# Performance work log

Hardware: AMD Instinct MI355X
Metric: run time of the kernel (lower is better)

The kernel has to match this reference:

```python
import jax, jax.numpy as jnp
import numpy as np

NUM_HEADS = 16
NUM_HIDDENS = 1024
D_K = NUM_HIDDENS // NUM_HEADS
NEG_INF = -1.0e9


def setup_inputs() -> dict:
    key = jax.random.key(0)
    kx, kq, kk, kv, ko, kl = jax.random.split(key, 6)
    B, S, D = 2, 2048, NUM_HIDDENS
    scale = 1.0 / np.sqrt(D)
    return {
        "X": jax.random.normal(kx, (B, S, D), dtype=jnp.float32),
        "valid_lens": jax.random.randint(kl, (B,), 0, S, dtype=jnp.int64),
        "W_q": jax.random.normal(kq, (D, D), dtype=jnp.float32) * scale,
        "W_k": jax.random.normal(kk, (D, D), dtype=jnp.float32) * scale,
        "W_v": jax.random.normal(kv, (D, D), dtype=jnp.float32) * scale,
        "W_o": jax.random.normal(ko, (D, D), dtype=jnp.float32) * scale,
    }


def _split_heads(x):
    # [B, S, D] -> [B, H, S, d_k]
    B, S, _ = x.shape
    return x.reshape(B, S, NUM_HEADS, D_K).transpose(0, 2, 1, 3)


def reference(X, valid_lens, W_q, W_k, W_v, W_o):
    B, S, D = X.shape
    # nn.Linear(bias=False): y = x @ W.T  (W is [out, in])
    Q = _split_heads(jnp.einsum("bsd,ed->bse", X, W_q))  # [B,H,S,dk]
    K = _split_heads(jnp.einsum("bsd,ed->bse", X, W_k))
    V = _split_heads(jnp.einsum("bsd,ed->bse", X, W_v))

    scores = jnp.einsum("bhqd,bhkd->bhqk", Q, K) / jnp.sqrt(
        jnp.asarray(D_K, dtype=X.dtype)
    )  # [B,H,S,S]

    # key-position mask per batch: positions >= valid_len get -1e9
    mask = jnp.arange(S)[None, :] >= valid_lens[:, None]  # [B,S]
    scores = jnp.where(mask[:, None, None, :], jnp.asarray(NEG_INF, X.dtype), scores)

    attn = jax.nn.softmax(scores, axis=-1)  # dropout p=0 -> identity
    out = jnp.einsum("bhqk,bhkd->bhqd", attn, V)  # [B,H,S,dk]
    out = out.transpose(0, 2, 1, 3).reshape(B, S, D)
    return jnp.einsum("bsd,ed->bse", out, W_o)
```

## Files before the change

kernel.cpp:

```cpp
#include <hip/hip_runtime.h>
#include <stdint.h>

#define S_LEN 2048
#define BATCH 2
#define DMODEL 1024
#define NHEAD 16
#define DK 64
#define MROWS (BATCH * S_LEN)

typedef __attribute__((ext_vector_type(8))) short bf16x8;
typedef __attribute__((ext_vector_type(4))) float f32x4;
typedef __attribute__((ext_vector_type(4))) short short4v;
typedef __attribute__((ext_vector_type(2))) uint32_t u32x2;

__device__ __forceinline__ short f2b(float f) {
    union { float f; uint32_t u; } c; c.f = f;
    uint32_t u = c.u;
    return (short)((u + 0x7fffu + ((u >> 16) & 1u)) >> 16);
}

__device__ __forceinline__ void gload16(const void* g, void* l) {
    __builtin_amdgcn_global_load_lds(
        (const __attribute__((address_space(1))) void*)g,
        (__attribute__((address_space(3))) void*)l, 16, 0, 0);
}

__global__ void cvt_kernel(const float* __restrict__ X, const float* __restrict__ Wq,
                           const float* __restrict__ Wk, const float* __restrict__ Wv,
                           const float* __restrict__ Wo,
                           short* __restrict__ Xb, short* __restrict__ Wqb,
                           short* __restrict__ Wkb, short* __restrict__ Wvb,
                           short* __restrict__ Wob) {
    const float* src; short* dst; int n4;
    switch (blockIdx.y) {
        case 0:  src = X;  dst = Xb;  n4 = MROWS * DMODEL / 4;  break;
        case 1:  src = Wq; dst = Wqb; n4 = DMODEL * DMODEL / 4; break;
        case 2:  src = Wk; dst = Wkb; n4 = DMODEL * DMODEL / 4; break;
        case 3:  src = Wv; dst = Wvb; n4 = DMODEL * DMODEL / 4; break;
        default: src = Wo; dst = Wob; n4 = DMODEL * DMODEL / 4; break;
    }
    for (int i = blockIdx.x * blockDim.x + threadIdx.x; i < n4;
         i += gridDim.x * blockDim.x) {
        float4 v = ((const float4*)src)[i];
        short4v o;
        o[0] = f2b(v.x); o[1] = f2b(v.y); o[2] = f2b(v.z); o[3] = f2b(v.w);
        ((short4v*)dst)[i] = o;
    }
}

template <int OUT_F32>
__global__ __launch_bounds__(256) void gemm_bt(
    const short* __restrict__ A,
    const short* __restrict__ Bt0, const short* __restrict__ Bt1,
    const short* __restrict__ Bt2,
    short* __restrict__ Cb0, short* __restrict__ Cb1, short* __restrict__ Cb2,
    float* __restrict__ Cf, int M, int N, int K) {
    __shared__ short sA[128 * 32];
    __shared__ short sB[128 * 32];

    const short* Bt = Bt0;
    short* Cb = Cb0;
    if (blockIdx.z == 1) { Bt = Bt1; Cb = Cb1; }
    else if (blockIdx.z == 2) { Bt = Bt2; Cb = Cb2; }

    const int tid = threadIdx.x;
    const int lane = tid & 63;
    const int wid = tid >> 6;
    const int wr = wid >> 1, wc = wid & 1;
    const int brow = blockIdx.y * 128;
    const int bcol = blockIdx.x * 128;
    const int lr = lane & 15;
    const int kh = (lane >> 4) << 3;

    f32x4 acc[4][4] = {};

    const int idx0 = tid, idx1 = tid + 256;
    const int ar0 = idx0 >> 2, ak0 = (idx0 & 3) << 3;
    const int ar1 = idx1 >> 2, ak1 = (idx1 & 3) << 3;

    const int nk = K >> 5;
    for (int kt = 0; kt < nk; ++kt) {
        __syncthreads();
        const int k0 = kt << 5;
        gload16(A + (size_t)(brow + ar0) * K + k0 + ak0, &sA[idx0 * 8]);
        gload16(A + (size_t)(brow + ar1) * K + k0 + ak1, &sA[idx1 * 8]);
        gload16(Bt + (size_t)(bcol + ar0) * K + k0 + ak0, &sB[idx0 * 8]);
        gload16(Bt + (size_t)(bcol + ar1) * K + k0 + ak1, &sB[idx1 * 8]);
        __syncthreads();

        bf16x8 a[4], b[4];
#pragma unroll
        for (int mt = 0; mt < 4; ++mt)
            a[mt] = *(const bf16x8*)&sA[(wr * 64 + mt * 16 + lr) * 32 + kh];
#pragma unroll
        for (int nt = 0; nt < 4; ++nt)
            b[nt] = *(const bf16x8*)&sB[(wc * 64 + nt * 16 + lr) * 32 + kh];
#pragma unroll
        for (int mt = 0; mt < 4; ++mt)
#pragma unroll
            for (int nt = 0; nt < 4; ++nt)
                acc[mt][nt] = __builtin_amdgcn_mfma_f32_16x16x32_bf16(
                    a[mt], b[nt], acc[mt][nt], 0, 0, 0);
    }

    const int rbase = (lane >> 4) << 2;
    const bool vtrans = (!OUT_F32) && (blockIdx.z == 2);
#pragma unroll
    for (int mt = 0; mt < 4; ++mt) {
#pragma unroll
        for (int nt = 0; nt < 4; ++nt) {
            if (vtrans) {
                int row0 = brow + wr * 64 + mt * 16 + rbase;
                int col = bcol + wc * 64 + nt * 16 + lr;
                int bb = row0 >> 11, key = row0 & 2047;
                int hh = col >> 6, d = col & 63;
                short4v pk;
#pragma unroll
                for (int j = 0; j < 4; ++j) pk[j] = f2b(acc[mt][nt][j]);
                *(short4v*)&Cb[((size_t)((bb * 16 + hh) * 64 + d)) * S_LEN + key] = pk;
            } else {
#pragma unroll
                for (int j = 0; j < 4; ++j) {
                    int row = brow + wr * 64 + mt * 16 + rbase + j;
                    int col = bcol + wc * 64 + nt * 16 + lr;
                    if (OUT_F32)
                        Cf[(size_t)row * N + col] = acc[mt][nt][j];
                    else
                        Cb[(size_t)row * N + col] = f2b(acc[mt][nt][j]);
                }
            }
        }
    }
}

__global__ __launch_bounds__(256) void attn_kernel(
    const short* __restrict__ Q, const short* __restrict__ K,
    const short* __restrict__ Vt, short* __restrict__ O,
    const int* __restrict__ vlens) {
    __shared__ short sK[2][64 * 64];
    __shared__ short sV[2][64 * 64];
    __shared__ short sP[4][16 * 64];

    const int tid = threadIdx.x;
    const int lane = tid & 63;
    const int w = tid >> 6;
    const int id = blockIdx.x;
    const int id2 = ((id & 7) << 7) | (id >> 3);
    const int qb = id2 & 31;
    const int bhx = id2 >> 5;
    const int b = bhx & 1, h = bhx >> 1;
    const int lr = lane & 15;
    const int kh = (lane >> 4) << 3;
    const int rbase = (lane >> 4) << 2;
    const int swq = (lr & 7) << 3;

    int vl = vlens[b];
    if (vl < 0) vl = 0;
    if (vl > S_LEN) vl = S_LEN;
    const bool allm = (vl == 0);
    if (allm) vl = S_LEN;
    const int nT = (vl + 63) >> 6;
    const int nFull = ((vl & 63) == 0) ? nT : nT - 1;

    const size_t rowbase = (size_t)(b * S_LEN) * DMODEL + h * DK;
    const short* vt = Vt + ((size_t)((b * 16 + h) * 64)) * S_LEN;

    const short* qrow = Q + rowbase + (size_t)(qb * 64 + w * 16 + lr) * DMODEL;
    bf16x8 qf0 = *(const bf16x8*)(qrow + kh);
    bf16x8 qf1 = *(const bf16x8*)(qrow + 32 + kh);
    if (allm) {
#pragma unroll
        for (int i = 0; i < 8; ++i) { qf0[i] = 0; qf1[i] = 0; }
    }

    f32x4 oac[4] = {};
    float m_run = -1e30f, m_c = -1e30f, l_run = 0.f;
    const float CEXP = 0.18033688011112042f;
    const float THRADD = 44.361419556f;

    const int lofs0 = lr * 64 + (kh ^ swq);
    const int lofs1 = lr * 64 + ((32 + kh) ^ swq);

    const int kr0 = tid >> 3;
    const int kr1 = kr0 + 32;
    const int kc0 = (((tid & 7) ^ (kr0 & 7)) << 3);
    const int kc1 = (((tid & 7) ^ (kr1 & 7)) << 3);

    const short* kA = K + rowbase + (size_t)kr0 * DMODEL + kc0;
    const short* kB = K + rowbase + (size_t)kr1 * DMODEL + kc1;
    const short* vA = vt + (size_t)kr0 * S_LEN + kc0;
    const short* vB = vt + (size_t)kr1 * S_LEN + kc1;

    gload16(kA, &sK[0][tid * 8]);
    gload16(kB, &sK[0][(tid + 256) * 8]);
    gload16(vA, &sV[0][tid * 8]);
    gload16(vB, &sV[0][(tid + 256) * 8]);
    __syncthreads();

#define TILE_BODY(MASKED_C)                                                     \
    do {                                                                        \
        constexpr bool MASKED = MASKED_C;                                       \
        const short* sKc = sK[cur];                                             \
        const short* sVc = sV[cur];                                             \
        const short* kL0 = sKc + lofs0;                                         \
        const short* kL1 = sKc + lofs1;                                         \
        f32x4 sacc[4] = {};                                                     \
        __builtin_amdgcn_s_setprio(1);                                          \
        _Pragma("unroll")                                                       \
        for (int nt = 0; nt < 4; ++nt) {                                        \
            bf16x8 kb0 = *(const bf16x8*)&kL0[nt * 1024];                       \
            bf16x8 kb1 = *(const bf16x8*)&kL1[nt * 1024];                       \
            sacc[nt] = __builtin_amdgcn_mfma_f32_16x16x32_bf16(                 \
                kb0, qf0, sacc[nt], 0, 0, 0);                                   \
            sacc[nt] = __builtin_amdgcn_mfma_f32_16x16x32_bf16(                 \
                kb1, qf1, sacc[nt], 0, 0, 0);                                   \
        }                                                                       \
        __builtin_amdgcn_s_setprio(0);                                          \
        if (MASKED) {                                                           \
            _Pragma("unroll")                                                   \
            for (int nt = 0; nt < 4; ++nt)                                      \
                _Pragma("unroll")                                               \
                for (int j = 0; j < 4; ++j) {                                   \
                    int keyi = t * 64 + nt * 16 + rbase + j;                    \
                    if (keyi >= vl) sacc[nt][j] = -3.0e38f;                     \
                }                                                               \
        }                                                                       \
        float t0 = fmaxf(fmaxf(sacc[0][0], sacc[0][1]), sacc[0][2]);            \
        float t1 = fmaxf(fmaxf(sacc[0][3], sacc[1][0]), sacc[1][1]);            \
        float t2 = fmaxf(fmaxf(sacc[1][2], sacc[1][3]), sacc[2][0]);            \
        float t3 = fmaxf(fmaxf(sacc[2][1], sacc[2][2]), sacc[2][3]);            \
        float t4 = fmaxf(fmaxf(sacc[3][0], sacc[3][1]), sacc[3][2]);            \
        float pmax = fmaxf(fmaxf(fmaxf(t0, t1), t2),                            \
                           fmaxf(fmaxf(t3, t4), sacc[3][3]));                   \
        if (__any(pmax > m_run + THRADD)) {                                     \
            float mx = pmax;                                                    \
            mx = fmaxf(mx, __shfl_xor(mx, 16));                                 \
            mx = fmaxf(mx, __shfl_xor(mx, 32));                                 \
            float scl = __builtin_exp2f((m_run - mx) * CEXP);                   \
            m_run = mx;                                                         \
            m_c = mx * CEXP;                                                    \
            l_run *= scl;                                                       \
            _Pragma("unroll")                                                   \
            for (int dt = 0; dt < 4; ++dt)                                      \
                _Pragma("unroll")                                               \
                for (int j = 0; j < 4; ++j) oac[dt][j] *= scl;                  \
        }                                                                       \
        float p[16];                                                            \
        _Pragma("unroll")                                                       \
        for (int nt = 0; nt < 4; ++nt)                                          \
            _Pragma("unroll")                                                   \
            for (int j = 0; j < 4; ++j)                                         \
                p[nt * 4 + j] = __builtin_exp2f(                                \
                    __builtin_fmaf(sacc[nt][j], CEXP, -m_c));                   \
        float ls = ((p[0] + p[1]) + (p[2] + p[3])) +                            \
                   ((p[4] + p[5]) + (p[6] + p[7]));                             \
        ls += ((p[8] + p[9]) + (p[10] + p[11])) +                               \
              ((p[12] + p[13]) + (p[14] + p[15]));                              \
        l_run += ls;                                                            \
        _Pragma("unroll")                                                       \
        for (int nt = 0; nt < 4; ++nt) {                                        \
            u32x2 r;                                                            \
            asm("v_cvt_pk_bf16_f32 %0, %1, %2"                                  \
                : "=v"(r[0]) : "v"(p[nt * 4 + 0]), "v"(p[nt * 4 + 1]));         \
            asm("v_cvt_pk_bf16_f32 %0, %1, %2"                                  \
                : "=v"(r[1]) : "v"(p[nt * 4 + 2]), "v"(p[nt * 4 + 3]));         \
            *(u32x2*)&sP[w][lr * 64 + ((nt * 16 + rbase) ^ swq)] = r;           \
        }                                                                       \
        const short* pL0 = &sP[w][lofs0];                                       \
        const short* pL1 = &sP[w][lofs1];                                       \
        const short* vL0 = sVc + lofs0;                                         \
        const short* vL1 = sVc + lofs1;                                         \
        __builtin_amdgcn_s_setprio(1);                                          \
        {                                                                       \
            bf16x8 pf0 = *(const bf16x8*)pL0;                                   \
            _Pragma("unroll")                                                   \
            for (int dt = 0; dt < 4; ++dt) {                                    \
                bf16x8 vf = *(const bf16x8*)&vL0[dt * 1024];                    \
                oac[dt] = __builtin_amdgcn_mfma_f32_16x16x32_bf16(              \
                    vf, pf0, oac[dt], 0, 0, 0);                                 \
            }                                                                   \
            bf16x8 pf1 = *(const bf16x8*)pL1;                                   \
            _Pragma("unroll")                                                   \
            for (int dt = 0; dt < 4; ++dt) {                                    \
                bf16x8 vf = *(const bf16x8*)&vL1[dt * 1024];                    \
                oac[dt] = __builtin_amdgcn_mfma_f32_16x16x32_bf16(              \
                    vf, pf1, oac[dt], 0, 0, 0);                                 \
            }                                                                   \
        }                                                                       \
        __builtin_amdgcn_s_setprio(0);                                          \
    } while (0)

    int cur = 0;
    for (int t = 0; t < nT; ++t) {
        const bool hn = (t + 1 < nT);
        if (hn) {
            short* sKn = sK[cur ^ 1];
            short* sVn = sV[cur ^ 1];
            kA += 64 * DMODEL; kB += 64 * DMODEL;
            vA += 64; vB += 64;
            gload16(kA, &sKn[tid * 8]);
            gload16(kB, &sKn[(tid + 256) * 8]);
            gload16(vA, &sVn[tid * 8]);
            gload16(vB, &sVn[(tid + 256) * 8]);
        }

        if (t < nFull) TILE_BODY(false);
        else TILE_BODY(true);

        __syncthreads();
        cur ^= 1;
    }
#undef TILE_BODY

    float lt = l_run + __shfl_xor(l_run, 16);
    lt += __shfl_xor(lt, 32);
    float rl = 1.f / lt;

    short* orow = O + rowbase + (size_t)(qb * 64 + w * 16 + lr) * DMODEL;
#pragma unroll
    for (int dt = 0; dt < 4; ++dt) {
        short4v pk;
#pragma unroll
        for (int j = 0; j < 4; ++j) pk[j] = f2b(oac[dt][j] * rl);
        *(short4v*)&orow[dt * 16 + rbase] = pk;
    }
}

extern "C" void kernel_launch(void* const* d_in, const int* in_sizes, int n_in,
                              void* d_out, int out_size, void* d_ws, size_t ws_size,
                              hipStream_t stream) {
    const float* X = (const float*)d_in[0];
    const int* vlens = (const int*)d_in[1];
    const float* Wq = (const float*)d_in[2];
    const float* Wk = (const float*)d_in[3];
    const float* Wv = (const float*)d_in[4];
    const float* Wo = (const float*)d_in[5];
    float* out = (float*)d_out;

    short* Xb = (short*)d_ws;
    short* Wqb = Xb + (size_t)MROWS * DMODEL;
    short* Wkb = Wqb + (size_t)DMODEL * DMODEL;
    short* Wvb = Wkb + (size_t)DMODEL * DMODEL;
    short* Wob = Wvb + (size_t)DMODEL * DMODEL;
    short* Qb = Wob + (size_t)DMODEL * DMODEL;
    short* Kb = Qb + (size_t)MROWS * DMODEL;
    short* Vtb = Kb + (size_t)MROWS * DMODEL;
    short* Ob = Vtb + (size_t)MROWS * DMODEL;

    cvt_kernel<<<dim3(512, 5), 256, 0, stream>>>(X, Wq, Wk, Wv, Wo, Xb, Wqb, Wkb,
                                                 Wvb, Wob);
    gemm_bt<0><<<dim3(8, 32, 3), 256, 0, stream>>>(Xb, Wqb, Wkb, Wvb, Qb, Kb, Vtb,
                                                   nullptr, MROWS, DMODEL, DMODEL);
    attn_kernel<<<dim3(1024), 256, 0, stream>>>(Qb, Kb, Vtb, Ob, vlens);
    gemm_bt<1><<<dim3(8, 32, 1), 256, 0, stream>>>(Ob, Wob, Wob, Wob, nullptr,
                                                   nullptr, nullptr, out, MROWS,
                                                   DMODEL, DMODEL);
}
```

Baseline: 119.7 us.

## Process 32 query rows per wave in attention and swizzle GEMM LDS

The attention kernel now gives each wave two 16-row query fragments, so every K and V tile loaded into LDS feeds twice as many MFMAs, and the grid is halved to 512 blocks. Softmax logic moves into a macro applied to both fragments, with separate running max/sum state and a doubled P buffer. Separately, the GEMM LDS layout gets an XOR swizzle on the k-offset to reduce bank conflicts on fragment reads. The cost is higher register pressure and fewer blocks for the 256 CUs, which may leave some idle or hurt load balance across varying valid lengths.

```diff
diff --git a/kernel.cpp b/kernel.cpp
--- a/kernel.cpp
+++ b/kernel.cpp
@@ -71,12 +71,14 @@
     const int bcol = blockIdx.x * 128;
     const int lr = lane & 15;
     const int kh = (lane >> 4) << 3;
+    const int swg = ((lr >> 1) & 3) << 3;
+    const int khs = kh ^ swg;
 
     f32x4 acc[4][4] = {};
 
     const int idx0 = tid, idx1 = tid + 256;
-    const int ar0 = idx0 >> 2, ak0 = (idx0 & 3) << 3;
-    const int ar1 = idx1 >> 2, ak1 = (idx1 & 3) << 3;
+    const int ar0 = idx0 >> 2, ak0 = ((idx0 & 3) << 3) ^ (((ar0 >> 1) & 3) << 3);
+    const int ar1 = idx1 >> 2, ak1 = ((idx1 & 3) << 3) ^ (((ar1 >> 1) & 3) << 3);
 
     const int nk = K >> 5;
     for (int kt = 0; kt < nk; ++kt) {
@@ -91,10 +93,10 @@
         bf16x8 a[4], b[4];
 #pragma unroll
         for (int mt = 0; mt < 4; ++mt)
-            a[mt] = *(const bf16x8*)&sA[(wr * 64 + mt * 16 + lr) * 32 + kh];
+            a[mt] = *(const bf16x8*)&sA[(wr * 64 + mt * 16 + lr) * 32 + khs];
 #pragma unroll
         for (int nt = 0; nt < 4; ++nt)
-            b[nt] = *(const bf16x8*)&sB[(wc * 64 + nt * 16 + lr) * 32 + kh];
+            b[nt] = *(const bf16x8*)&sB[(wc * 64 + nt * 16 + lr) * 32 + khs];
 #pragma unroll
         for (int mt = 0; mt < 4; ++mt)
 #pragma unroll
@@ -139,15 +141,15 @@
     const int* __restrict__ vlens) {
     __shared__ short sK[2][64 * 64];
     __shared__ short sV[2][64 * 64];
-    __shared__ short sP[4][16 * 64];
+    __shared__ short sP[4][2][16 * 64];
 
     const int tid = threadIdx.x;
     const int lane = tid & 63;
     const int w = tid >> 6;
     const int id = blockIdx.x;
-    const int id2 = ((id & 7) << 7) | (id >> 3);
-    const int qb = id2 & 31;
-    const int bhx = id2 >> 5;
+    const int id2 = ((id & 7) << 6) | (id >> 3);
+    const int qb = id2 & 15;
+    const int bhx = id2 >> 4;
     const int b = bhx & 1, h = bhx >> 1;
     const int lr = lane & 15;
     const int kh = (lane >> 4) << 3;
@@ -165,16 +167,20 @@
     const size_t rowbase = (size_t)(b * S_LEN) * DMODEL + h * DK;
     const short* vt = Vt + ((size_t)((b * 16 + h) * 64)) * S_LEN;
 
-    const short* qrow = Q + rowbase + (size_t)(qb * 64 + w * 16 + lr) * DMODEL;
-    bf16x8 qf0 = *(const bf16x8*)(qrow + kh);
-    bf16x8 qf1 = *(const bf16x8*)(qrow + 32 + kh);
+    const short* qrowA = Q + rowbase + (size_t)(qb * 128 + w * 32 + lr) * DMODEL;
+    const short* qrowB = qrowA + 16 * DMODEL;
+    bf16x8 qf0a = *(const bf16x8*)(qrowA + kh);
+    bf16x8 qf1a = *(const bf16x8*)(qrowA + 32 + kh);
+    bf16x8 qf0b = *(const bf16x8*)(qrowB + kh);
+    bf16x8 qf1b = *(const bf16x8*)(qrowB + 32 + kh);
     if (allm) {
 #pragma unroll
-        for (int i = 0; i < 8; ++i) { qf0[i] = 0; qf1[i] = 0; }
-    }
-
-    f32x4 oac[4] = {};
-    float m_run = -1e30f, m_c = -1e30f, l_run = 0.f;
+        for (int i = 0; i < 8; ++i) { qf0a[i] = 0; qf1a[i] = 0; qf0b[i] = 0; qf1b[i] = 0; }
+    }
+
+    f32x4 oacA[4] = {}, oacB[4] = {};
+    float mA = -1e30f, mcA = -1e30f, lA = 0.f;
+    float mB = -1e30f, mcB = -1e30f, lB = 0.f;
     const float CEXP = 0.18033688011112042f;
     const float THRADD = 44.361419556f;
 
@@ -196,6 +202,51 @@
     gload16(vA, &sV[0][tid * 8]);
     gload16(vB, &sV[0][(tid + 256) * 8]);
     __syncthreads();
+
+#define SOFTMAX_FRAG(SACC, MRUN, MC, LRUN, OAC, SPW)                            \
+    do {                                                                        \
+        float t0 = fmaxf(fmaxf(SACC[0][0], SACC[0][1]), SACC[0][2]);            \
+        float t1 = fmaxf(fmaxf(SACC[0][3], SACC[1][0]), SACC[1][1]);            \
+        float t2 = fmaxf(fmaxf(SACC[1][2], SACC[1][3]), SACC[2][0]);            \
+        float t3 = fmaxf(fmaxf(SACC[2][1], SACC[2][2]), SACC[2][3]);            \
+        float t4 = fmaxf(fmaxf(SACC[3][0], SACC[3][1]), SACC[3][2]);            \
+        float pmax = fmaxf(fmaxf(fmaxf(t0, t1), t2),                            \
+                           fmaxf(fmaxf(t3, t4), SACC[3][3]));                   \
+        if (__any(pmax > MRUN + THRADD)) {                                      \
+            float mx = pmax;                                                    \
+            mx = fmaxf(mx, __shfl_xor(mx, 16));                                 \
+            mx = fmaxf(mx, __shfl_xor(mx, 32));                                 \
+            float scl = __builtin_exp2f((MRUN - mx) * CEXP);                    \
+            MRUN = mx;                                                          \
+            MC = mx * CEXP;                                                     \
+            LRUN *= scl;                                                        \
+            _Pragma("unroll")                                                   \
+            for (int dt = 0; dt < 4; ++dt)                                      \
+                _Pragma("unroll")                                               \
+                for (int j = 0; j < 4; ++j) OAC[dt][j] *= scl;                  \
+        }                                                                       \
+        float p[16];                                                            \
+        _Pragma("unroll")                                                       \
+        for (int nt = 0; nt < 4; ++nt)                                          \
+            _Pragma("unroll")                                                   \
+            for (int j = 0; j < 4; ++j)                                         \
+                p[nt * 4 + j] = __builtin_exp2f(                                \
+                    __builtin_fmaf(SACC[nt][j], CEXP, -MC));                    \
+        float ls = ((p[0] + p[1]) + (p[2] + p[3])) +                            \
+                   ((p[4] + p[5]) + (p[6] + p[7]));                             \
+        ls += ((p[8] + p[9]) + (p[10] + p[11])) +                               \
+              ((p[12] + p[13]) + (p[14] + p[15]));                              \
+        LRUN += ls;                                                             \
+        _Pragma("unroll")                                                       \
+        for (int nt = 0; nt < 4; ++nt) {                                        \
+            u32x2 r;                                                            \
+            asm("v_cvt_pk_bf16_f32 %0, %1, %2"                                  \
+                : "=v"(r[0]) : "v"(p[nt * 4 + 0]), "v"(p[nt * 4 + 1]));         \
+            asm("v_cvt_pk_bf16_f32 %0, %1, %2"                                  \
+                : "=v"(r[1]) : "v"(p[nt * 4 + 2]), "v"(p[nt * 4 + 3]));         \
+            *(u32x2*)&SPW[lr * 64 + ((nt * 16 + rbase) ^ swq)] = r;             \
+        }                                                                       \
+    } while (0)
 
 #define TILE_BODY(MASKED_C)                                                     \
     do {                                                                        \
@@ -204,16 +255,20 @@
         const short* sVc = sV[cur];                                             \
         const short* kL0 = sKc + lofs0;                                         \
         const short* kL1 = sKc + lofs1;                                         \
-        f32x4 sacc[4] = {};                                                     \
+        f32x4 saccA[4] = {}, saccB[4] = {};                                     \
         __builtin_amdgcn_s_setprio(1);                                          \
         _Pragma("unroll")                                                       \
         for (int nt = 0; nt < 4; ++nt) {                                        \
             bf16x8 kb0 = *(const bf16x8*)&kL0[nt * 1024];                       \
             bf16x8 kb1 = *(const bf16x8*)&kL1[nt * 1024];                       \
-            sacc[nt] = __builtin_amdgcn_mfma_f32_16x16x32_bf16(                 \
-                kb0, qf0, sacc[nt], 0, 0, 0);                                   \
-            sacc[nt] = __builtin_amdgcn_mfma_f32_16x16x32_bf16(                 \
-                kb1, qf1, sacc[nt], 0, 0, 0);                                   \
+            saccA[nt] = __builtin_amdgcn_mfma_f32_16x16x32_bf16(                \
+                kb0, qf0a, saccA[nt], 0, 0, 0);                                 \
+            saccB[nt] = __builtin_amdgcn_mfma_f32_16x16x32_bf16(                \
+                kb0, qf0b, saccB[nt], 0, 0, 0);                                 \
+            saccA[nt] = __builtin_amdgcn_mfma_f32_16x16x32_bf16(                \
+                kb1, qf1a, saccA[nt], 0, 0, 0);                                 \
+            saccB[nt] = __builtin_amdgcn_mfma_f32_16x16x32_bf16(                \
+                kb1, qf1b, saccB[nt], 0, 0, 0);                                 \
         }                                                                       \
         __builtin_amdgcn_s_setprio(0);                                          \
         if (MASKED) {                                                           \
@@ -222,69 +277,35 @@
                 _Pragma("unroll")                                               \
                 for (int j = 0; j < 4; ++j) {                                   \
                     int keyi = t * 64 + nt * 16 + rbase + j;                    \
-                    if (keyi >= vl) sacc[nt][j] = -3.0e38f;                     \
+                    if (keyi >= vl) { saccA[nt][j] = -3.0e38f;                  \
+                                      saccB[nt][j] = -3.0e38f; }                \
                 }                                                               \
         }                                                                       \
-        float t0 = fmaxf(fmaxf(sacc[0][0], sacc[0][1]), sacc[0][2]);            \
-        float t1 = fmaxf(fmaxf(sacc[0][3], sacc[1][0]), sacc[1][1]);            \
-        float t2 = fmaxf(fmaxf(sacc[1][2], sacc[1][3]), sacc[2][0]);            \
-        float t3 = fmaxf(fmaxf(sacc[2][1], sacc[2][2]), sacc[2][3]);            \
-        float t4 = fmaxf(fmaxf(sacc[3][0], sacc[3][1]), sacc[3][2]);            \
-        float pmax = fmaxf(fmaxf(fmaxf(t0, t1), t2),                            \
-                           fmaxf(fmaxf(t3, t4), sacc[3][3]));                   \
-        if (__any(pmax > m_run + THRADD)) {                                     \
-            float mx = pmax;                                                    \
-            mx = fmaxf(mx, __shfl_xor(mx, 16));                                 \
-            mx = fmaxf(mx, __shfl_xor(mx, 32));                                 \
-            float scl = __builtin_exp2f((m_run - mx) * CEXP);                   \
-            m_run = mx;                                                         \
-            m_c = mx * CEXP;                                                    \
-            l_run *= scl;                                                       \
-            _Pragma("unroll")                                                   \
-            for (int dt = 0; dt < 4; ++dt)                                      \
-                _Pragma("unroll")                                               \
-                for (int j = 0; j < 4; ++j) oac[dt][j] *= scl;                  \
-        }                                                                       \
-        float p[16];                                                            \
-        _Pragma("unroll")                                                       \
-        for (int nt = 0; nt < 4; ++nt)                                          \
-            _Pragma("unroll")                                                   \
-            for (int j = 0; j < 4; ++j)                                         \
-                p[nt * 4 + j] = __builtin_exp2f(                                \
-                    __builtin_fmaf(sacc[nt][j], CEXP, -m_c));                   \
-        float ls = ((p[0] + p[1]) + (p[2] + p[3])) +                            \
-                   ((p[4] + p[5]) + (p[6] + p[7]));                             \
-        ls += ((p[8] + p[9]) + (p[10] + p[11])) +                               \
-              ((p[12] + p[13]) + (p[14] + p[15]));                              \
-        l_run += ls;                                                            \
-        _Pragma("unroll")                                                       \
-        for (int nt = 0; nt < 4; ++nt) {                                        \
-            u32x2 r;                                                            \
-            asm("v_cvt_pk_bf16_f32 %0, %1, %2"                                  \
-                : "=v"(r[0]) : "v"(p[nt * 4 + 0]), "v"(p[nt * 4 + 1]));         \
-            asm("v_cvt_pk_bf16_f32 %0, %1, %2"                                  \
-                : "=v"(r[1]) : "v"(p[nt * 4 + 2]), "v"(p[nt * 4 + 3]));         \
-            *(u32x2*)&sP[w][lr * 64 + ((nt * 16 + rbase) ^ swq)] = r;           \
-        }                                                                       \
-        const short* pL0 = &sP[w][lofs0];                                       \
-        const short* pL1 = &sP[w][lofs1];                                       \
+        SOFTMAX_FRAG(saccA, mA, mcA, lA, oacA, (&sP[w][0][0]));                 \
+        SOFTMAX_FRAG(saccB, mB, mcB, lB, oacB, (&sP[w][1][0]));                 \
         const short* vL0 = sVc + lofs0;                                         \
         const short* vL1 = sVc + lofs1;                                         \
         __builtin_amdgcn_s_setprio(1);                                          \
         {                                                                       \
-            bf16x8 pf0 = *(const bf16x8*)pL0;                                   \
+            bf16x8 pfA = *(const bf16x8*)&sP[w][0][lofs0];                      \
+            bf16x8 pfB = *(const bf16x8*)&sP[w][1][lofs0];                      \
             _Pragma("unroll")                                                   \
             for (int dt = 0; dt < 4; ++dt) {                                    \
                 bf16x8 vf = *(const bf16x8*)&vL0[dt * 1024];                    \
-                oac[dt] = __builtin_amdgcn_mfma_f32_16x16x32_bf16(              \
-                    vf, pf0, oac[dt], 0, 0, 0);                                 \
+                oacA[dt] = __builtin_amdgcn_mfma_f32_16x16x32_bf16(             \
+                    vf, pfA, oacA[dt], 0, 0, 0);                                \
+                oacB[dt] = __builtin_amdgcn_mfma_f32_16x16x32_bf16(             \
+                    vf, pfB, oacB[dt], 0, 0, 0);                                \
             }                                                                   \
-            bf16x8 pf1 = *(const bf16x8*)pL1;                                   \
+            pfA = *(const bf16x8*)&sP[w][0][lofs1];                             \
+            pfB = *(const bf16x8*)&sP[w][1][lofs1];                             \
             _Pragma("unroll")                                                   \
             for (int dt = 0; dt < 4; ++dt) {                                    \
                 bf16x8 vf = *(const bf16x8*)&vL1[dt * 1024];                    \
-                oac[dt] = __builtin_amdgcn_mfma_f32_16x16x32_bf16(              \
-                    vf, pf1, oac[dt], 0, 0, 0);                                 \
+                oacA[dt] = __builtin_amdgcn_mfma_f32_16x16x32_bf16(             \
+                    vf, pfA, oacA[dt], 0, 0, 0);                                \
+                oacB[dt] = __builtin_amdgcn_mfma_f32_16x16x32_bf16(             \
+                    vf, pfB, oacB[dt], 0, 0, 0);                                \
             }                                                                   \
         }                                                                       \
         __builtin_amdgcn_s_setprio(0);                                          \
@@ -311,18 +332,27 @@
         cur ^= 1;
     }
 #undef TILE_BODY
-
-    float lt = l_run + __shfl_xor(l_run, 16);
-    lt += __shfl_xor(lt, 32);
-    float rl = 1.f / lt;
-
-    short* orow = O + rowbase + (size_t)(qb * 64 + w * 16 + lr) * DMODEL;
+#undef SOFTMAX_FRAG
+
+    float ltA = lA + __shfl_xor(lA, 16);
+    ltA += __shfl_xor(ltA, 32);
+    float rlA = 1.f / ltA;
+    float ltB = lB + __shfl_xor(lB, 16);
+    ltB += __shfl_xor(ltB, 32);
+    float rlB = 1.f / ltB;
+
+    short* orowA = O + rowbase + (size_t)(qb * 128 + w * 32 + lr) * DMODEL;
+    short* orowB = orowA + 16 * DMODEL;
 #pragma unroll
     for (int dt = 0; dt < 4; ++dt) {
-        short4v pk;
-#pragma unroll
-        for (int j = 0; j < 4; ++j) pk[j] = f2b(oac[dt][j] * rl);
-        *(short4v*)&orow[dt * 16 + rbase] = pk;
+        short4v pkA, pkB;
+#pragma unroll
+        for (int j = 0; j < 4; ++j) {
+            pkA[j] = f2b(oacA[dt][j] * rlA);
+            pkB[j] = f2b(oacB[dt][j] * rlB);
+        }
+        *(short4v*)&orowA[dt * 16 + rbase] = pkA;
+        *(short4v*)&orowB[dt * 16 + rbase] = pkB;
     }
 }
 
@@ -351,7 +381,7 @@
                                                  Wvb, Wob);
     gemm_bt<0><<<dim3(8, 32, 3), 256, 0, stream>>>(Xb, Wqb, Wkb, Wvb, Qb, Kb, Vtb,
                                                    nullptr, MROWS, DMODEL, DMODEL);
-    attn_kernel<<<dim3(1024), 256, 0, stream>>>(Qb, Kb, Vtb, Ob, vlens);
+    attn_kernel<<<dim3(512), 256, 0, stream>>>(Qb, Kb, Vtb, Ob, vlens);
     gemm_bt<1><<<dim3(8, 32, 1), 256, 0, stream>>>(Ob, Wob, Wob, Wob, nullptr,
                                                    nullptr, nullptr, out, MROWS,
                                                    DMODEL, DMODEL);
```

Result: faster. 116.6 us (-2.6%).
